# Kernel tuning notes

Measured on AMD Instinct MI355X. Metric: run time of the kernel, lower is better.

## Reference

```python
import jax, jax.numpy as jnp
import numpy as np

EPS = 1e-08
NUM_EMBEDDINGS = 8192
EMBEDDING_DIM = 256
N_TOKENS = 32768


def setup_inputs() -> dict:
    key = jax.random.key(0)
    k1, k2, k3 = jax.random.split(key, 3)
    input_data = jax.random.normal(k1, (N_TOKENS, EMBEDDING_DIM), dtype=jnp.float32)
    rand = jax.random.normal(k2, (N_TOKENS, EMBEDDING_DIM), dtype=jnp.float32)
    codebooks = jax.random.normal(k3, (NUM_EMBEDDINGS, EMBEDDING_DIM), dtype=jnp.float32)
    return {"input_data": input_data, "rand": rand, "codebooks": codebooks}


def reference(input_data, rand, codebooks):
    # d2: (N, K) -- this full matrix is what a fused kernel would avoid.
    d2 = (jnp.sum(input_data * input_data, axis=1, keepdims=True)
          - 2.0 * input_data @ codebooks.T
          + jnp.sum(codebooks * codebooks, axis=1)[None, :])
    min_idx = jnp.argmin(d2, axis=1)                      # (N,)
    hard_q = codebooks[min_idx]                           # (N, D)

    # Noise substitution: scale unit-ish gaussian noise to the residual norm.
    r_norm = jnp.linalg.norm(input_data - hard_q, axis=1, keepdims=True)
    n_norm = jnp.linalg.norm(rand, axis=1, keepdims=True)
    quantized_input = input_data + (r_norm / (n_norm + EPS)) * rand

    # Perplexity from codebook usage counts (no grad path in original).
    counts = jnp.zeros((NUM_EMBEDDINGS,), dtype=jnp.float32).at[min_idx].add(1.0)
    total = jnp.maximum(counts.sum(), 1.0)
    avg_probs = counts / total
    perplexity = jnp.exp(-jnp.sum(avg_probs * jnp.log(avg_probs + EPS)))
    num_unique_indices = jnp.sum(counts > 0).astype(jnp.int32)
    return quantized_input, perplexity, num_unique_indices
```

## Files before the change

kernel.cpp:

```cpp
#include <hip/hip_runtime.h>
#include <stdint.h>

#define N_TOKENS 32768
#define N_CODES  8192
#define DIM      256
#define EPSF     1e-8f

typedef __bf16 bf16x8 __attribute__((ext_vector_type(8)));
typedef float  f32x4  __attribute__((ext_vector_type(4)));

#define WS_CNORM_OFF  (4u*1024u*1024u)
#define WS_HIST_OFF   (WS_CNORM_OFF + N_CODES*4u)

__global__ __launch_bounds__(256) void k_prep(const float* __restrict__ cbf,
                                              unsigned short* __restrict__ cbh,
                                              float* __restrict__ cnorm,
                                              int* __restrict__ hist) {
    const int tid = blockIdx.x * 256 + threadIdx.x;
    if (tid < N_CODES) hist[tid] = 0;

    const int w = threadIdx.x >> 6;
    const int lane = threadIdx.x & 63;
    const int row = blockIdx.x * 4 + w;

    const float4 v = ((const float4*)(cbf + (size_t)row * DIM))[lane];
    float sq = v.x * v.x + v.y * v.y + v.z * v.z + v.w * v.w;

    ushort4 u;
    u.x = __builtin_bit_cast(unsigned short, (__bf16)v.x);
    u.y = __builtin_bit_cast(unsigned short, (__bf16)v.y);
    u.z = __builtin_bit_cast(unsigned short, (__bf16)v.z);
    u.w = __builtin_bit_cast(unsigned short, (__bf16)v.w);
    ((ushort4*)(cbh + (size_t)row * DIM))[lane] = u;

    #pragma unroll
    for (int d = 1; d < 64; d <<= 1) sq += __shfl_xor(sq, d);
    if (lane == 0) cnorm[row] = sq;
}

__global__ __launch_bounds__(512, 2) void k_argmin(const float* __restrict__ X,
                                                   const float* __restrict__ R,
                                                   const unsigned short* __restrict__ cbh,
                                                   const float* __restrict__ cnorm,
                                                   float* __restrict__ out,
                                                   int* __restrict__ hist) {
    __shared__ __attribute__((aligned(16))) char smem[87040];
    float* cnS   = (float*)(smem + 65536);
    float* redv  = (float*)(smem + 66048);
    int*   redi  = (int*)(smem + 68096);
    float* maxvS = (float*)(smem + 70144);

    const int tid  = threadIdx.x;
    const int w    = tid >> 6;
    const int lane = tid & 63;
    const int lr   = lane & 15;
    const int lq   = lane >> 4;
    const int th   = w >> 2;
    const int wc   = w & 3;
    const int r0   = blockIdx.x * 128;
    const int mycol = wc * 16 + lr;

    {
        const float4* Xf4 = (const float4*)(X + (size_t)(r0 + 16 * w) * DIM);
        #pragma unroll
        for (int i = 0; i < 16; ++i) {
            const float4 v = Xf4[i * 64 + lane];
            ushort4 u;
            u.x = __builtin_bit_cast(unsigned short, (__bf16)v.x);
            u.y = __builtin_bit_cast(unsigned short, (__bf16)v.y);
            u.z = __builtin_bit_cast(unsigned short, (__bf16)v.z);
            u.w = __builtin_bit_cast(unsigned short, (__bf16)v.w);
            *(ushort4*)(smem + (16 * w + i) * 544 + lane * 8) = u;
        }
    }
    __syncthreads();

    bf16x8 A[4][8];
    #pragma unroll
    for (int mf = 0; mf < 4; ++mf)
        #pragma unroll
        for (int kc = 0; kc < 8; ++kc)
            A[mf][kc] = *(const bf16x8*)(smem + (64 * th + mf * 16 + lr) * 544 + kc * 64 + lq * 16);
    __syncthreads();

    const int half = lane >> 5, l5 = lane & 31;
    int srcoff[4];
    #pragma unroll
    for (int s = 0; s < 4; ++s) {
        const int c = 8 * w + 2 * s + half;
        const int j = (l5 - c) & 31;
        srcoff[s] = c * 512 + j * 16;
    }
    const char* cbb = (const char*)cbh;

    #pragma unroll
    for (int s = 0; s < 4; ++s)
        __builtin_amdgcn_global_load_lds(
            (const __attribute__((address_space(1))) unsigned int*)(cbb + srcoff[s]),
            (__attribute__((address_space(3))) unsigned int*)(smem + w * 4096 + s * 1024),
            16, 0, 0);
    if (w == 0)
        __builtin_amdgcn_global_load_lds(
            (const __attribute__((address_space(1))) unsigned int*)(cnorm + lane),
            (__attribute__((address_space(3))) unsigned int*)(cnS),
            4, 0, 0);
    __syncthreads();

    float maxv[16];
    int   maxi[16];
    #pragma unroll
    for (int i = 0; i < 16; ++i) { maxv[i] = -3.4e38f; maxi[i] = 0; }

    for (int cc = 0; cc < 128; ++cc) {
        const int cur = (cc & 1) * 32768;
        if (cc + 1 < 128) {
            const int nxt = ((cc + 1) & 1) * 32768;
            const char* src = cbb + (size_t)(cc + 1) * 32768;
            #pragma unroll
            for (int s = 0; s < 4; ++s)
                __builtin_amdgcn_global_load_lds(
                    (const __attribute__((address_space(1))) unsigned int*)(src + srcoff[s]),
                    (__attribute__((address_space(3))) unsigned int*)(smem + nxt + w * 4096 + s * 1024),
                    16, 0, 0);
            if (w == 0)
                __builtin_amdgcn_global_load_lds(
                    (const __attribute__((address_space(1))) unsigned int*)(cnorm + (cc + 1) * 64 + lane),
                    (__attribute__((address_space(3))) unsigned int*)(cnS + ((cc + 1) & 1) * 64),
                    4, 0, 0);
        }

        const float cinit = -0.5f * cnS[(cc & 1) * 64 + mycol];
        f32x4 acc[4];
        #pragma unroll
        for (int mf = 0; mf < 4; ++mf) {
            acc[mf][0] = cinit; acc[mf][1] = cinit; acc[mf][2] = cinit; acc[mf][3] = cinit;
        }

        #pragma unroll
        for (int kc = 0; kc < 8; ++kc) {
            const bf16x8 b = *(const bf16x8*)(smem + cur + mycol * 512 +
                                              (((kc * 4 + lq + mycol) & 31) << 4));
            #pragma unroll
            for (int mf = 0; mf < 4; ++mf)
                acc[mf] = __builtin_amdgcn_mfma_f32_16x16x32_bf16(A[mf][kc], b, acc[mf], 0, 0, 0);
        }

        const int col = cc * 64 + mycol;
        #pragma unroll
        for (int mf = 0; mf < 4; ++mf)
            #pragma unroll
            for (int r = 0; r < 4; ++r) {
                const float v = acc[mf][r];
                const int j = mf * 4 + r;
                if (v > maxv[j]) { maxv[j] = v; maxi[j] = col; }
            }

        __syncthreads();
    }

    #pragma unroll
    for (int mf = 0; mf < 4; ++mf)
        #pragma unroll
        for (int r = 0; r < 4; ++r) {
            float v = maxv[mf * 4 + r]; int ix = maxi[mf * 4 + r];
            #pragma unroll
            for (int d = 1; d <= 8; d <<= 1) {
                const float ov = __shfl_xor(v, d);
                const int   oi = __shfl_xor(ix, d);
                if (ov > v || (ov == v && oi < ix)) { v = ov; ix = oi; }
            }
            if (lr == 0) {
                const int row = mf * 16 + lq * 4 + r;
                redv[w * 64 + row] = v; redi[w * 64 + row] = ix;
            }
        }
    __syncthreads();

    if (tid < 128) {
        const int t = tid, tth = t >> 6, tl = t & 63;
        float v = redv[(4 * tth) * 64 + tl]; int ix = redi[(4 * tth) * 64 + tl];
        #pragma unroll
        for (int ww = 1; ww < 4; ++ww) {
            const float ov = redv[(4 * tth + ww) * 64 + tl];
            const int   oi = redi[(4 * tth + ww) * 64 + tl];
            if (ov > v || (ov == v && oi < ix)) { v = ov; ix = oi; }
        }
        maxvS[t] = v;
        atomicAdd(&hist[ix], 1);
    }
    __syncthreads();

    for (int i = 0; i < 16; ++i) {
        const int tl = 16 * w + i;
        const int tok = r0 + tl;
        const float4 x = ((const float4*)(X + (size_t)tok * DIM))[lane];
        const float4 r = ((const float4*)(R + (size_t)tok * DIM))[lane];

        float x2 = x.x * x.x + x.y * x.y + x.z * x.z + x.w * x.w;
        float n2 = r.x * r.x + r.y * r.y + r.z * r.z + r.w * r.w;
        #pragma unroll
        for (int d = 1; d < 64; d <<= 1) {
            x2 += __shfl_xor(x2, d);
            n2 += __shfl_xor(n2, d);
        }
        const float mv = maxvS[tl];
        const float d2 = fmaxf(fmaf(-2.f, mv, x2), 0.f);
        const float s = sqrtf(d2) / (sqrtf(n2) + EPSF);

        float4 o;
        o.x = fmaf(s, r.x, x.x);
        o.y = fmaf(s, r.y, x.y);
        o.z = fmaf(s, r.z, x.z);
        o.w = fmaf(s, r.w, x.w);
        ((float4*)(out + (size_t)tok * DIM))[lane] = o;
    }
}

__global__ __launch_bounds__(1024) void k_stats(const int* __restrict__ hist,
                                                float* __restrict__ outs) {
    float s = 0.f; int u = 0;
    for (int b = threadIdx.x; b < N_CODES; b += 1024) {
        const float c = (float)hist[b];
        if (c > 0.f) ++u;
        const float p = c * (1.f / (float)N_TOKENS);
        s += p * logf(p + EPSF);
    }
    #pragma unroll
    for (int d = 1; d < 64; d <<= 1) {
        s += __shfl_xor(s, d);
        u += __shfl_xor(u, d);
    }
    __shared__ float ss[16];
    __shared__ int   su[16];
    const int w = threadIdx.x >> 6, lane = threadIdx.x & 63;
    if (lane == 0) { ss[w] = s; su[w] = u; }
    __syncthreads();
    if (threadIdx.x == 0) {
        float st = 0.f; int ut = 0;
        #pragma unroll
        for (int i = 0; i < 16; ++i) { st += ss[i]; ut += su[i]; }
        outs[0] = expf(-st);
        outs[1] = (float)ut;
    }
}

extern "C" void kernel_launch(void* const* d_in, const int* in_sizes, int n_in,
                              void* d_out, int out_size, void* d_ws, size_t ws_size,
                              hipStream_t stream) {
    const float* X = (const float*)d_in[0];
    const float* R = (const float*)d_in[1];
    const float* C = (const float*)d_in[2];
    float* out = (float*)d_out;

    char* ws = (char*)d_ws;
    unsigned short* cbh = (unsigned short*)ws;
    float* cnorm = (float*)(ws + WS_CNORM_OFF);
    int*   hist  = (int*)(ws + WS_HIST_OFF);

    k_prep  <<<N_CODES / 4,    256, 0, stream>>>(C, cbh, cnorm, hist);
    k_argmin<<<N_TOKENS / 128, 512, 0, stream>>>(X, R, cbh, cnorm, out, hist);
    k_stats <<<1, 1024, 0, stream>>>(hist, out + (size_t)N_TOKENS * DIM);
}
```

Before: 244.8 us.

## Fuse prep, argmin and stats into one cooperative kernel with grid syncs

Merges the codebook conversion/norm kernel, the argmin kernel and the stats kernel into a single cooperative launch of 256 blocks, using grid-wide syncs in place of kernel boundaries. It also restructures the codebook chunk loop to interleave two accumulator sets, so the argmin epilogue of one chunk overlaps the MFMAs of the next. The aim is to remove two launch gaps and the tail of the single-block stats kernel. In exchange it adds grid-sync costs, relies on all 256 blocks being co-resident, and uses more registers for the second accumulator.

New measurement: 411.3 us. +68.0%, slower.

```diff
diff --git a/kernel.cpp b/kernel.cpp
--- a/kernel.cpp
+++ b/kernel.cpp
@@ -1,5 +1,8 @@
 #include <hip/hip_runtime.h>
+#include <hip/hip_cooperative_groups.h>
 #include <stdint.h>
+
+namespace cg = cooperative_groups;
 
 #define N_TOKENS 32768
 #define N_CODES  8192
@@ -12,38 +15,13 @@
 #define WS_CNORM_OFF  (4u*1024u*1024u)
 #define WS_HIST_OFF   (WS_CNORM_OFF + N_CODES*4u)
 
-__global__ __launch_bounds__(256) void k_prep(const float* __restrict__ cbf,
-                                              unsigned short* __restrict__ cbh,
-                                              float* __restrict__ cnorm,
-                                              int* __restrict__ hist) {
-    const int tid = blockIdx.x * 256 + threadIdx.x;
-    if (tid < N_CODES) hist[tid] = 0;
-
-    const int w = threadIdx.x >> 6;
-    const int lane = threadIdx.x & 63;
-    const int row = blockIdx.x * 4 + w;
-
-    const float4 v = ((const float4*)(cbf + (size_t)row * DIM))[lane];
-    float sq = v.x * v.x + v.y * v.y + v.z * v.z + v.w * v.w;
-
-    ushort4 u;
-    u.x = __builtin_bit_cast(unsigned short, (__bf16)v.x);
-    u.y = __builtin_bit_cast(unsigned short, (__bf16)v.y);
-    u.z = __builtin_bit_cast(unsigned short, (__bf16)v.z);
-    u.w = __builtin_bit_cast(unsigned short, (__bf16)v.w);
-    ((ushort4*)(cbh + (size_t)row * DIM))[lane] = u;
-
-    #pragma unroll
-    for (int d = 1; d < 64; d <<= 1) sq += __shfl_xor(sq, d);
-    if (lane == 0) cnorm[row] = sq;
-}
-
-__global__ __launch_bounds__(512, 2) void k_argmin(const float* __restrict__ X,
-                                                   const float* __restrict__ R,
-                                                   const unsigned short* __restrict__ cbh,
-                                                   const float* __restrict__ cnorm,
-                                                   float* __restrict__ out,
-                                                   int* __restrict__ hist) {
+__global__ __launch_bounds__(512, 2) void k_fused(const float* __restrict__ X,
+                                                  const float* __restrict__ R,
+                                                  const float* __restrict__ Cf,
+                                                  unsigned short* __restrict__ cbh,
+                                                  float* __restrict__ cnorm,
+                                                  float* __restrict__ out,
+                                                  int* __restrict__ hist) {
     __shared__ __attribute__((aligned(16))) char smem[87040];
     float* cnS   = (float*)(smem + 65536);
     float* redv  = (float*)(smem + 66048);
@@ -60,6 +38,27 @@
     const int r0   = blockIdx.x * 128;
     const int mycol = wc * 16 + lr;
 
+    cg::grid_group grid = cg::this_grid();
+
+    if (tid < 32) hist[blockIdx.x * 32 + tid] = 0;
+    #pragma unroll
+    for (int i = 0; i < 4; ++i) {
+        const int row = blockIdx.x * 32 + w * 4 + i;
+        const float4 v = ((const float4*)(Cf + (size_t)row * DIM))[lane];
+        float sq = v.x * v.x + v.y * v.y + v.z * v.z + v.w * v.w;
+        ushort4 u;
+        u.x = __builtin_bit_cast(unsigned short, (__bf16)v.x);
+        u.y = __builtin_bit_cast(unsigned short, (__bf16)v.y);
+        u.z = __builtin_bit_cast(unsigned short, (__bf16)v.z);
+        u.w = __builtin_bit_cast(unsigned short, (__bf16)v.w);
+        ((ushort4*)(cbh + (size_t)row * DIM))[lane] = u;
+        #pragma unroll
+        for (int d = 1; d < 64; d <<= 1) sq += __shfl_xor(sq, d);
+        if (lane == 0) cnorm[row] = sq;
+    }
+    __threadfence();
+    grid.sync();
+
     {
         const float4* Xf4 = (const float4*)(X + (size_t)(r0 + 16 * w) * DIM);
         #pragma unroll
@@ -93,58 +92,43 @@
     }
     const char* cbb = (const char*)cbh;
 
-    #pragma unroll
-    for (int s = 0; s < 4; ++s)
-        __builtin_amdgcn_global_load_lds(
-            (const __attribute__((address_space(1))) unsigned int*)(cbb + srcoff[s]),
-            (__attribute__((address_space(3))) unsigned int*)(smem + w * 4096 + s * 1024),
-            16, 0, 0);
-    if (w == 0)
-        __builtin_amdgcn_global_load_lds(
-            (const __attribute__((address_space(1))) unsigned int*)(cnorm + lane),
-            (__attribute__((address_space(3))) unsigned int*)(cnS),
-            4, 0, 0);
-    __syncthreads();
+    auto stage_chunk = [&](int chunk) {
+        const char* src = cbb + (size_t)chunk * 32768;
+        const int buf = (chunk & 1) * 32768;
+        #pragma unroll
+        for (int s = 0; s < 4; ++s)
+            __builtin_amdgcn_global_load_lds(
+                (const __attribute__((address_space(1))) unsigned int*)(src + srcoff[s]),
+                (__attribute__((address_space(3))) unsigned int*)(smem + buf + w * 4096 + s * 1024),
+                16, 0, 0);
+        if (w == 0)
+            __builtin_amdgcn_global_load_lds(
+                (const __attribute__((address_space(1))) unsigned int*)(cnorm + chunk * 64 + lane),
+                (__attribute__((address_space(3))) unsigned int*)(cnS + (chunk & 1) * 64),
+                4, 0, 0);
+    };
 
     float maxv[16];
     int   maxi[16];
     #pragma unroll
     for (int i = 0; i < 16; ++i) { maxv[i] = -3.4e38f; maxi[i] = 0; }
 
-    for (int cc = 0; cc < 128; ++cc) {
-        const int cur = (cc & 1) * 32768;
-        if (cc + 1 < 128) {
-            const int nxt = ((cc + 1) & 1) * 32768;
-            const char* src = cbb + (size_t)(cc + 1) * 32768;
-            #pragma unroll
-            for (int s = 0; s < 4; ++s)
-                __builtin_amdgcn_global_load_lds(
-                    (const __attribute__((address_space(1))) unsigned int*)(src + srcoff[s]),
-                    (__attribute__((address_space(3))) unsigned int*)(smem + nxt + w * 4096 + s * 1024),
-                    16, 0, 0);
-            if (w == 0)
-                __builtin_amdgcn_global_load_lds(
-                    (const __attribute__((address_space(1))) unsigned int*)(cnorm + (cc + 1) * 64 + lane),
-                    (__attribute__((address_space(3))) unsigned int*)(cnS + ((cc + 1) & 1) * 64),
-                    4, 0, 0);
-        }
-
-        const float cinit = -0.5f * cnS[(cc & 1) * 64 + mycol];
-        f32x4 acc[4];
+    auto mfma_chunk = [&](f32x4* acc, int bufbase, int cnbase) {
+        const float cinit = -0.5f * cnS[cnbase + mycol];
         #pragma unroll
         for (int mf = 0; mf < 4; ++mf) {
             acc[mf][0] = cinit; acc[mf][1] = cinit; acc[mf][2] = cinit; acc[mf][3] = cinit;
         }
-
         #pragma unroll
         for (int kc = 0; kc < 8; ++kc) {
-            const bf16x8 b = *(const bf16x8*)(smem + cur + mycol * 512 +
+            const bf16x8 b = *(const bf16x8*)(smem + bufbase + mycol * 512 +
                                               (((kc * 4 + lq + mycol) & 31) << 4));
             #pragma unroll
             for (int mf = 0; mf < 4; ++mf)
                 acc[mf] = __builtin_amdgcn_mfma_f32_16x16x32_bf16(A[mf][kc], b, acc[mf], 0, 0, 0);
         }
-
+    };
+    auto epi_chunk = [&](const f32x4* acc, int cc) {
         const int col = cc * 64 + mycol;
         #pragma unroll
         for (int mf = 0; mf < 4; ++mf)
@@ -154,9 +138,24 @@
                 const int j = mf * 4 + r;
                 if (v > maxv[j]) { maxv[j] = v; maxi[j] = col; }
             }
-
+    };
+
+    stage_chunk(0);
+    __syncthreads();
+
+    f32x4 accA[4], accB[4];
+    for (int cp = 0; cp < 64; ++cp) {
+        const int c0 = 2 * cp, c1 = 2 * cp + 1;
+        stage_chunk(c1);
+        mfma_chunk(accA, 0, 0);
+        if (cp > 0) epi_chunk(accB, c0 - 1);
         __syncthreads();
-    }
+        if (cp < 63) stage_chunk(c1 + 1);
+        mfma_chunk(accB, 32768, 64);
+        epi_chunk(accA, c0);
+        __syncthreads();
+    }
+    epi_chunk(accB, 127);
 
     #pragma unroll
     for (int mf = 0; mf < 4; ++mf)
@@ -214,33 +213,34 @@
         o.w = fmaf(s, r.w, x.w);
         ((float4*)(out + (size_t)tok * DIM))[lane] = o;
     }
-}
-
-__global__ __launch_bounds__(1024) void k_stats(const int* __restrict__ hist,
-                                                float* __restrict__ outs) {
-    float s = 0.f; int u = 0;
-    for (int b = threadIdx.x; b < N_CODES; b += 1024) {
-        const float c = (float)hist[b];
-        if (c > 0.f) ++u;
-        const float p = c * (1.f / (float)N_TOKENS);
-        s += p * logf(p + EPSF);
-    }
-    #pragma unroll
-    for (int d = 1; d < 64; d <<= 1) {
-        s += __shfl_xor(s, d);
-        u += __shfl_xor(u, d);
-    }
-    __shared__ float ss[16];
-    __shared__ int   su[16];
-    const int w = threadIdx.x >> 6, lane = threadIdx.x & 63;
-    if (lane == 0) { ss[w] = s; su[w] = u; }
-    __syncthreads();
-    if (threadIdx.x == 0) {
-        float st = 0.f; int ut = 0;
-        #pragma unroll
-        for (int i = 0; i < 16; ++i) { st += ss[i]; ut += su[i]; }
-        outs[0] = expf(-st);
-        outs[1] = (float)ut;
+
+    __threadfence();
+    grid.sync();
+    if (blockIdx.x == 0) {
+        float s = 0.f; int u = 0;
+        for (int b = tid; b < N_CODES; b += 512) {
+            const int ci = __hip_atomic_load(hist + b, __ATOMIC_RELAXED,
+                                             __HIP_MEMORY_SCOPE_AGENT);
+            if (ci > 0) ++u;
+            const float p = (float)ci * (1.f / (float)N_TOKENS);
+            s += p * logf(p + EPSF);
+        }
+        #pragma unroll
+        for (int d = 1; d < 64; d <<= 1) {
+            s += __shfl_xor(s, d);
+            u += __shfl_xor(u, d);
+        }
+        float* ss = (float*)smem;
+        int*   su = (int*)(smem + 64);
+        if (lane == 0) { ss[w] = s; su[w] = u; }
+        __syncthreads();
+        if (tid == 0) {
+            float st = 0.f; int ut = 0;
+            #pragma unroll
+            for (int i = 0; i < 8; ++i) { st += ss[i]; ut += su[i]; }
+            out[(size_t)N_TOKENS * DIM]     = expf(-st);
+            out[(size_t)N_TOKENS * DIM + 1] = (float)ut;
+        }
     }
 }
 
@@ -257,7 +257,7 @@
     float* cnorm = (float*)(ws + WS_CNORM_OFF);
     int*   hist  = (int*)(ws + WS_HIST_OFF);
 
-    k_prep  <<<N_CODES / 4,    256, 0, stream>>>(C, cbh, cnorm, hist);
-    k_argmin<<<N_TOKENS / 128, 512, 0, stream>>>(X, R, cbh, cnorm, out, hist);
-    k_stats <<<1, 1024, 0, stream>>>(hist, out + (size_t)N_TOKENS * DIM);
+    void* args[] = { (void*)&X, (void*)&R, (void*)&C, (void*)&cbh,
+                     (void*)&cnorm, (void*)&out, (void*)&hist };
+    hipLaunchCooperativeKernel(k_fused, dim3(256), dim3(512), args, 0, stream);
 }
```
